# Kernel optimization log

Hardware: AMD Instinct MI355X
Metric: run time of the kernel (lower is better)

Reference implementation:

```python
import jax, jax.numpy as jnp
import numpy as np

N = 4096
TAU = 0.2          # args.tau relaxation temperature
EPS = 1e-10        # numerical guard for logit of clamped probs


def setup_inputs() -> dict:
    key = jax.random.key(0)
    k1, k2, k3 = jax.random.split(key, 3)
    r = jax.random.uniform(k1, (N, N))
    ori_adj = jnp.where(r < 0.005, -1.0, jnp.where(r < 0.01, 1.0, 0.0)).astype(jnp.float32)
    # nn.init.uniform_(change_links_prob, 0.0, 0.001)
    change_links_prob = jax.random.uniform(k2, (N, N), minval=0.0, maxval=0.001, dtype=jnp.float32)
    # uniform noise for the RelaxedBernoulli logistic reparameterization
    u = jax.random.uniform(k3, (N, N), minval=1e-6, maxval=1.0 - 1e-6, dtype=jnp.float32)
    return {"ori_adj": ori_adj, "change_links_prob": change_links_prob, "u": u}


def reference(ori_adj, change_links_prob, u):
    # --- get_modified_adj: RelaxedBernoulliStraightThrough(tau, clamp(p,0,1)).rsample() ---
    p = jnp.clip(change_links_prob, EPS, 1.0 - EPS)      # torch.clamp(p, 0, 1) + logit guard
    logits = jnp.log(p) - jnp.log1p(-p)
    noise = jnp.log(u) - jnp.log1p(-u)                   # logistic noise
    soft = jax.nn.sigmoid((logits + noise) / TAU)        # relaxed sample
    hard = jnp.round(soft)                               # quantized sample
    change_prob = soft + jax.lax.stop_gradient(hard - soft)  # straight-through
    mod_adj = ori_adj + change_prob * (-2.0 * ori_adj)   # ori_adj * (1 - 2*b)

    # --- balance_degree_directed(mod_adj) ---
    # torch.diag(matrix) returns the diagonal VECTOR, broadcast-subtracted per row (faithful).
    A = mod_adj + mod_adj.T - jnp.diag(mod_adj)
    A_abs = jnp.abs(A)
    tr3 = jnp.einsum('ij,jk,ki->', A, A, A)              # trace(A @ A @ A)
    tr3_abs = jnp.einsum('ij,jk,ki->', A_abs, A_abs, A_abs)
    balance = 0.5 * (1.0 + tr3 / tr3_abs)
    return mod_adj, balance
```

## Files before the change

kernel.cpp:

```cpp
#include <hip/hip_runtime.h>
#include <hip/hip_bf16.h>
#include <cstdint>
#include <cstddef>

#define N 4096
#define NN ((size_t)N * (size_t)N)

typedef int   int4v   __attribute__((ext_vector_type(4)));
typedef float float4v __attribute__((ext_vector_type(4)));

__device__ inline void async16(const void* g, void* lds) {
    __builtin_amdgcn_global_load_lds(
        (const __attribute__((address_space(1))) void*)g,
        (__attribute__((address_space(3))) void*)lds, 16, 0, 0);
}

__global__ __launch_bounds__(512) void fused_mod_build(
        const float* __restrict__ ori,
        const float* __restrict__ clp,
        const float* __restrict__ uu,
        float* __restrict__ out,
        signed char* __restrict__ A,
        signed char* __restrict__ AT,
        signed char* __restrict__ Aa,
        signed char* __restrict__ ATa,
        double* __restrict__ accs) {
    const int I = blockIdx.x, J = blockIdx.y;
    if (I > J) return;
    __shared__ float sm1[64][65];
    __shared__ float sm2[64][65];
    __shared__ float dI[64], dJ[64];
    const int t    = threadIdx.x;
    const int half = t >> 8;
    const int tt   = t & 255;
    const int r    = tt >> 2;
    const int q    = tt & 3;
    const int bi = I * 64, bj = J * 64;
    if (I == 0 && J == 0 && t < 2) accs[t] = 0.0;
    if (t < 128) {
        const int x = (t < 64) ? (bi + t) : (bj + (t - 64));
        const size_t off = (size_t)x * N + x;
        const float o = ori[off];
        const float hard = (clp[off] + uu[off] >= 1.0f) ? 1.0f : 0.0f;
        const float d = fmaf(hard, -2.0f * o, o);
        if (t < 64) dI[t] = d; else dJ[t - 64] = d;
    }
    {
        const int rowbase = half ? bj : bi;
        const int colbase = half ? bi : bj;
        float (*sm)[65] = half ? sm2 : sm1;
        const bool wr = (half == 0) || (I != J);
        #pragma unroll
        for (int k = 0; k < 4; ++k) {
            const size_t off = (size_t)(rowbase + r) * N + colbase + k * 16 + q * 4;
            const float4v o4 = *(const float4v*)(ori + off);
            const float4v p4 = *(const float4v*)(clp + off);
            const float4v u4 = *(const float4v*)(uu + off);
            float4v m;
            #pragma unroll
            for (int c = 0; c < 4; ++c) {
                const float hard = (p4[c] + u4[c] >= 1.0f) ? 1.0f : 0.0f;
                m[c] = fmaf(hard, -2.0f * o4[c], o4[c]);
                sm[r][k * 16 + q * 4 + c] = m[c];
            }
            if (wr) *(float4v*)(out + off) = m;
        }
    }
    __syncthreads();
    if (half == 0) {
        int pkA1[4], pkAa1[4], pkT1[4], pkTa1[4];
        #pragma unroll
        for (int w = 0; w < 4; ++w) {
            int a1w = 0, aa1w = 0, t1w = 0, ta1w = 0;
            #pragma unroll
            for (int k = 0; k < 4; ++k) {
                const int c = q * 16 + w * 4 + k;
                const float a1 = sm1[r][c] + sm2[c][r] - dJ[c];
                const int v1 = (int)a1;  const int u1 = v1 < 0 ? -v1 : v1;
                a1w  |= (v1 & 255) << (8 * k);
                aa1w |= (u1 & 255) << (8 * k);
                const float t1 = sm1[c][r] + sm2[r][c] - dJ[r];
                const int w1 = (int)t1;  const int x1 = w1 < 0 ? -w1 : w1;
                t1w  |= (w1 & 255) << (8 * k);
                ta1w |= (x1 & 255) << (8 * k);
            }
            pkA1[w] = a1w; pkAa1[w] = aa1w; pkT1[w] = t1w; pkTa1[w] = ta1w;
        }
        const size_t oIJ = (size_t)(bi + r) * N + bj + q * 16;
        const size_t oJI = (size_t)(bj + r) * N + bi + q * 16;
        *(int4v*)&A  [oIJ] = *(int4v*)pkA1;
        *(int4v*)&Aa [oIJ] = *(int4v*)pkAa1;
        *(int4v*)&AT [oJI] = *(int4v*)pkT1;
        *(int4v*)&ATa[oJI] = *(int4v*)pkTa1;
    } else if (I != J) {
        int pkA2[4], pkAa2[4], pkT2[4], pkTa2[4];
        #pragma unroll
        for (int w = 0; w < 4; ++w) {
            int a2w = 0, aa2w = 0, t2w = 0, ta2w = 0;
            #pragma unroll
            for (int k = 0; k < 4; ++k) {
                const int c = q * 16 + w * 4 + k;
                const float a2 = sm2[r][c] + sm1[c][r] - dI[c];
                const int v2 = (int)a2;  const int u2 = v2 < 0 ? -v2 : v2;
                a2w  |= (v2 & 255) << (8 * k);
                aa2w |= (u2 & 255) << (8 * k);
                const float t2 = sm2[c][r] + sm1[r][c] - dI[r];
                const int w2 = (int)t2;  const int x2 = w2 < 0 ? -w2 : w2;
                t2w  |= (w2 & 255) << (8 * k);
                ta2w |= (x2 & 255) << (8 * k);
            }
            pkA2[w] = a2w; pkAa2[w] = aa2w; pkT2[w] = t2w; pkTa2[w] = ta2w;
        }
        const size_t oIJ = (size_t)(bi + r) * N + bj + q * 16;
        const size_t oJI = (size_t)(bj + r) * N + bi + q * 16;
        *(int4v*)&A  [oJI] = *(int4v*)pkA2;
        *(int4v*)&Aa [oJI] = *(int4v*)pkAa2;
        *(int4v*)&AT [oIJ] = *(int4v*)pkT2;
        *(int4v*)&ATa[oIJ] = *(int4v*)pkTa2;
    }
}

#define BK 64
#define NT (N / BK)
#define BUFSZ 32768

__global__ __launch_bounds__(512, 2) void gemm_trace_i8(
        const signed char* __restrict__ Ag,
        const signed char* __restrict__ ATg,
        const signed char* __restrict__ Aag,
        const signed char* __restrict__ ATag,
        double* __restrict__ accs) {
    __shared__ __align__(16) signed char lds[4 * BUFSZ];
    __shared__ int red[8];
    const int z = blockIdx.z;
    const signed char* Asrc = z ? Aag  : Ag;
    const signed char* Bsrc = z ? ATag : ATg;
    const int i0 = blockIdx.y * 256;
    const int k0 = blockIdx.x * 256;
    const int t = threadIdx.x;
    const int lane = t & 63;
    const int wave = t >> 6;
    const int wm = wave >> 2;
    const int wn = wave & 3;
    const int quad = lane >> 4;
    const int col  = lane & 15;

    const int c1 = t;
    const int r1 = c1 >> 2;
    const int r2 = r1 + 128;
    const int s1 = (((c1 & 3) ^ ((r1 >> 1) & 3)) << 4);
    const int s2 = (((c1 & 3) ^ ((r2 >> 1) & 3)) << 4);
    const signed char* gA1 = Asrc + (size_t)(i0 + r1) * N + s1;
    const signed char* gA2 = Asrc + (size_t)(i0 + r2) * N + s2;
    const signed char* gB1 = Bsrc + (size_t)(k0 + r1) * N + s1;
    const signed char* gB2 = Bsrc + (size_t)(k0 + r2) * N + s2;
    const int ldsA1 = (wave * 64) * 16;
    const int ldsA2 = 8192  + (wave * 64) * 16;
    const int ldsB1 = 16384 + (wave * 64) * 16;
    const int ldsB2 = 24576 + (wave * 64) * 16;
    const int fsw = ((quad ^ ((col >> 1) & 3)) << 4);

    int4v acc[8][4];
    #pragma unroll
    for (int a = 0; a < 8; ++a)
        #pragma unroll
        for (int b = 0; b < 4; ++b)
            acc[a][b] = (int4v){0, 0, 0, 0};

    for (int p = 0; p < 3; ++p) {
        const int pb = p * BUFSZ;
        const size_t go = (size_t)p * BK;
        async16(gA1 + go, lds + pb + ldsA1);
        async16(gA2 + go, lds + pb + ldsA2);
        async16(gB1 + go, lds + pb + ldsB1);
        async16(gB2 + go, lds + pb + ldsB2);
    }
    asm volatile("s_waitcnt vmcnt(8)" ::: "memory");
    __builtin_amdgcn_s_barrier();
    __builtin_amdgcn_sched_barrier(0);

    for (int j = 0; j < NT; ++j) {
        const int buf = (j & 3) * BUFSZ;
        const signed char* Ab = lds + buf;
        const signed char* Bb = lds + buf + 16384;
        const int pre = j + 3;
        const size_t go = (size_t)pre * BK;
        const int pb = (pre & 3) * BUFSZ;
        int4v af0[4], af1[4], bf[4];
        #pragma unroll
        for (int tr = 0; tr < 4; ++tr)
            af0[tr] = *(const int4v*)(Ab + ((wm * 128 + tr * 16 + col) << 6) + fsw);
        #pragma unroll
        for (int tc = 0; tc < 4; ++tc)
            bf[tc] = *(const int4v*)(Bb + ((wn * 64 + tc * 16 + col) << 6) + fsw);
        #pragma unroll
        for (int tr = 0; tr < 4; ++tr)
            af1[tr] = *(const int4v*)(Ab + ((wm * 128 + 64 + tr * 16 + col) << 6) + fsw);
        if (pre < NT) {
            async16(gA1 + go, lds + pb + ldsA1);
            async16(gA2 + go, lds + pb + ldsA2);
            async16(gB1 + go, lds + pb + ldsB1);
            async16(gB2 + go, lds + pb + ldsB2);
        }
        asm volatile("s_waitcnt lgkmcnt(4)" ::: "memory");
        __builtin_amdgcn_sched_barrier(0);
        __builtin_amdgcn_s_setprio(1);
        #pragma unroll
        for (int tr = 0; tr < 4; ++tr)
            #pragma unroll
            for (int tc = 0; tc < 4; ++tc)
                acc[tr][tc] = __builtin_amdgcn_mfma_i32_16x16x64_i8(af0[tr], bf[tc], acc[tr][tc], 0, 0, 0);
        __builtin_amdgcn_s_setprio(0);
        asm volatile("s_waitcnt lgkmcnt(0)" ::: "memory");
        __builtin_amdgcn_sched_barrier(0);
        __builtin_amdgcn_s_setprio(1);
        #pragma unroll
        for (int tr = 0; tr < 4; ++tr)
            #pragma unroll
            for (int tc = 0; tc < 4; ++tc)
                acc[4 + tr][tc] = __builtin_amdgcn_mfma_i32_16x16x64_i8(af1[tr], bf[tc], acc[4 + tr][tc], 0, 0, 0);
        __builtin_amdgcn_s_setprio(0);
        if (j < NT - 3)       { asm volatile("s_waitcnt vmcnt(8)" ::: "memory"); }
        else if (j == NT - 3) { asm volatile("s_waitcnt vmcnt(4)" ::: "memory"); }
        else if (j == NT - 2) { asm volatile("s_waitcnt vmcnt(0)" ::: "memory"); }
        __builtin_amdgcn_s_barrier();
        __builtin_amdgcn_sched_barrier(0);
    }

    int part = 0;
    #pragma unroll
    for (int mr = 0; mr < 8; ++mr) {
        const int ib = i0 + wm * 128 + mr * 16 + quad * 4;
        #pragma unroll
        for (int tc = 0; tc < 4; ++tc) {
            const int kk = k0 + wn * 64 + tc * 16 + col;
            const int mv = *(const int*)&Asrc[(size_t)kk * N + ib];
            #pragma unroll
            for (int r = 0; r < 4; ++r)
                part += acc[mr][tc][r] * (int)(signed char)(mv >> (8 * r));
        }
    }
    #pragma unroll
    for (int off = 32; off > 0; off >>= 1)
        part += __shfl_down(part, off, 64);
    if (lane == 0) red[wave] = part;
    __syncthreads();
    if (t == 0) {
        int tot = 0;
        #pragma unroll
        for (int w = 0; w < 8; ++w) tot += red[w];
        atomicAdd(&accs[z], (double)tot);
    }
}

__global__ void finalize_kernel(const double* __restrict__ accs, float* __restrict__ out) {
    out[NN] = (float)(0.5 * (1.0 + accs[0] / accs[1]));
}

extern "C" void kernel_launch(void* const* d_in, const int* in_sizes, int n_in,
                              void* d_out, int out_size, void* d_ws, size_t ws_size,
                              hipStream_t stream) {
    const float* ori = (const float*)d_in[0];
    const float* clp = (const float*)d_in[1];
    const float* u   = (const float*)d_in[2];
    float* out = (float*)d_out;
    char* ws = (char*)d_ws;
    signed char* A8   = (signed char*)ws;
    signed char* AT8  = (signed char*)(ws + NN);
    signed char* Aa8  = (signed char*)(ws + 2 * NN);
    signed char* ATa8 = (signed char*)(ws + 3 * NN);
    double*      accs = (double*)(ws + 4 * NN);

    fused_mod_build<<<dim3(64, 64), 512, 0, stream>>>(
        ori, clp, u, out, A8, AT8, Aa8, ATa8, accs);
    gemm_trace_i8<<<dim3(N / 256, N / 256, 2), 512, 0, stream>>>(A8, AT8, Aa8, ATa8, accs);
    finalize_kernel<<<1, 1, 0, stream>>>(accs, out);
}
```

Before: 393.7 us.

## Compute abs GEMM from signed int8 tiles in-register, drop separate abs matrices

The build kernel now writes only the signed int8 matrix and its transpose, not separate absolute-value copies. The GEMM kernel computes byte-wise absolute values of the loaded fragments in registers and runs both the signed and absolute MFMA chains in one pass over shared tiles. This halves global int8 writes and GEMM operand loads, and the grid drops its z dimension. In exchange it doubles the accumulator registers (launch bounds change to one block per CU), adds ALU work per fragment, and it also batches the float loads in the build kernel.

```diff
diff --git a/kernel.cpp b/kernel.cpp
--- a/kernel.cpp
+++ b/kernel.cpp
@@ -13,6 +13,20 @@
     __builtin_amdgcn_global_load_lds(
         (const __attribute__((address_space(1))) void*)g,
         (__attribute__((address_space(3))) void*)lds, 16, 0, 0);
+}
+
+__device__ inline unsigned absb4(unsigned v) {
+    unsigned s = (v >> 7) & 0x01010101u;
+    unsigned m = s * 255u;
+    return (v ^ m) + s;
+}
+__device__ inline int4v absfrag(int4v v) {
+    int4v r;
+    r[0] = (int)absb4((unsigned)v[0]);
+    r[1] = (int)absb4((unsigned)v[1]);
+    r[2] = (int)absb4((unsigned)v[2]);
+    r[3] = (int)absb4((unsigned)v[3]);
+    return r;
 }
 
 __global__ __launch_bounds__(512) void fused_mod_build(
@@ -22,8 +36,6 @@
         float* __restrict__ out,
         signed char* __restrict__ A,
         signed char* __restrict__ AT,
-        signed char* __restrict__ Aa,
-        signed char* __restrict__ ATa,
         double* __restrict__ accs) {
     const int I = blockIdx.x, J = blockIdx.y;
     if (I > J) return;
@@ -50,73 +62,80 @@
         const int colbase = half ? bi : bj;
         float (*sm)[65] = half ? sm2 : sm1;
         const bool wr = (half == 0) || (I != J);
+        float4v o4[4], p4[4], u4[4];
         #pragma unroll
         for (int k = 0; k < 4; ++k) {
             const size_t off = (size_t)(rowbase + r) * N + colbase + k * 16 + q * 4;
-            const float4v o4 = *(const float4v*)(ori + off);
-            const float4v p4 = *(const float4v*)(clp + off);
-            const float4v u4 = *(const float4v*)(uu + off);
+            o4[k] = *(const float4v*)(ori + off);
+        }
+        #pragma unroll
+        for (int k = 0; k < 4; ++k) {
+            const size_t off = (size_t)(rowbase + r) * N + colbase + k * 16 + q * 4;
+            p4[k] = *(const float4v*)(clp + off);
+        }
+        #pragma unroll
+        for (int k = 0; k < 4; ++k) {
+            const size_t off = (size_t)(rowbase + r) * N + colbase + k * 16 + q * 4;
+            u4[k] = *(const float4v*)(uu + off);
+        }
+        #pragma unroll
+        for (int k = 0; k < 4; ++k) {
             float4v m;
             #pragma unroll
             for (int c = 0; c < 4; ++c) {
-                const float hard = (p4[c] + u4[c] >= 1.0f) ? 1.0f : 0.0f;
-                m[c] = fmaf(hard, -2.0f * o4[c], o4[c]);
+                const float hard = (p4[k][c] + u4[k][c] >= 1.0f) ? 1.0f : 0.0f;
+                m[c] = fmaf(hard, -2.0f * o4[k][c], o4[k][c]);
                 sm[r][k * 16 + q * 4 + c] = m[c];
             }
-            if (wr) *(float4v*)(out + off) = m;
+            if (wr) {
+                const size_t off = (size_t)(rowbase + r) * N + colbase + k * 16 + q * 4;
+                *(float4v*)(out + off) = m;
+            }
         }
     }
     __syncthreads();
     if (half == 0) {
-        int pkA1[4], pkAa1[4], pkT1[4], pkTa1[4];
+        int pkA1[4], pkT1[4];
         #pragma unroll
         for (int w = 0; w < 4; ++w) {
-            int a1w = 0, aa1w = 0, t1w = 0, ta1w = 0;
+            int a1w = 0, t1w = 0;
             #pragma unroll
             for (int k = 0; k < 4; ++k) {
                 const int c = q * 16 + w * 4 + k;
                 const float a1 = sm1[r][c] + sm2[c][r] - dJ[c];
-                const int v1 = (int)a1;  const int u1 = v1 < 0 ? -v1 : v1;
-                a1w  |= (v1 & 255) << (8 * k);
-                aa1w |= (u1 & 255) << (8 * k);
+                const int v1 = (int)a1;
+                a1w |= (v1 & 255) << (8 * k);
                 const float t1 = sm1[c][r] + sm2[r][c] - dJ[r];
-                const int w1 = (int)t1;  const int x1 = w1 < 0 ? -w1 : w1;
-                t1w  |= (w1 & 255) << (8 * k);
-                ta1w |= (x1 & 255) << (8 * k);
-            }
-            pkA1[w] = a1w; pkAa1[w] = aa1w; pkT1[w] = t1w; pkTa1[w] = ta1w;
+                const int w1 = (int)t1;
+                t1w |= (w1 & 255) << (8 * k);
+            }
+            pkA1[w] = a1w; pkT1[w] = t1w;
         }
         const size_t oIJ = (size_t)(bi + r) * N + bj + q * 16;
         const size_t oJI = (size_t)(bj + r) * N + bi + q * 16;
-        *(int4v*)&A  [oIJ] = *(int4v*)pkA1;
-        *(int4v*)&Aa [oIJ] = *(int4v*)pkAa1;
-        *(int4v*)&AT [oJI] = *(int4v*)pkT1;
-        *(int4v*)&ATa[oJI] = *(int4v*)pkTa1;
+        *(int4v*)&A [oIJ] = *(int4v*)pkA1;
+        *(int4v*)&AT[oJI] = *(int4v*)pkT1;
     } else if (I != J) {
-        int pkA2[4], pkAa2[4], pkT2[4], pkTa2[4];
+        int pkA2[4], pkT2[4];
         #pragma unroll
         for (int w = 0; w < 4; ++w) {
-            int a2w = 0, aa2w = 0, t2w = 0, ta2w = 0;
+            int a2w = 0, t2w = 0;
             #pragma unroll
             for (int k = 0; k < 4; ++k) {
                 const int c = q * 16 + w * 4 + k;
                 const float a2 = sm2[r][c] + sm1[c][r] - dI[c];
-                const int v2 = (int)a2;  const int u2 = v2 < 0 ? -v2 : v2;
-                a2w  |= (v2 & 255) << (8 * k);
-                aa2w |= (u2 & 255) << (8 * k);
+                const int v2 = (int)a2;
+                a2w |= (v2 & 255) << (8 * k);
                 const float t2 = sm2[c][r] + sm1[r][c] - dI[r];
-                const int w2 = (int)t2;  const int x2 = w2 < 0 ? -w2 : w2;
-                t2w  |= (w2 & 255) << (8 * k);
-                ta2w |= (x2 & 255) << (8 * k);
-            }
-            pkA2[w] = a2w; pkAa2[w] = aa2w; pkT2[w] = t2w; pkTa2[w] = ta2w;
+                const int w2 = (int)t2;
+                t2w |= (w2 & 255) << (8 * k);
+            }
+            pkA2[w] = a2w; pkT2[w] = t2w;
         }
         const size_t oIJ = (size_t)(bi + r) * N + bj + q * 16;
         const size_t oJI = (size_t)(bj + r) * N + bi + q * 16;
-        *(int4v*)&A  [oJI] = *(int4v*)pkA2;
-        *(int4v*)&Aa [oJI] = *(int4v*)pkAa2;
-        *(int4v*)&AT [oIJ] = *(int4v*)pkT2;
-        *(int4v*)&ATa[oIJ] = *(int4v*)pkTa2;
+        *(int4v*)&A [oJI] = *(int4v*)pkA2;
+        *(int4v*)&AT[oIJ] = *(int4v*)pkT2;
     }
 }
 
@@ -124,17 +143,14 @@
 #define NT (N / BK)
 #define BUFSZ 32768
 
-__global__ __launch_bounds__(512, 2) void gemm_trace_i8(
+__global__ __launch_bounds__(512, 1) void gemm_trace_i8(
         const signed char* __restrict__ Ag,
         const signed char* __restrict__ ATg,
-        const signed char* __restrict__ Aag,
-        const signed char* __restrict__ ATag,
         double* __restrict__ accs) {
     __shared__ __align__(16) signed char lds[4 * BUFSZ];
-    __shared__ int red[8];
-    const int z = blockIdx.z;
-    const signed char* Asrc = z ? Aag  : Ag;
-    const signed char* Bsrc = z ? ATag : ATg;
+    __shared__ int red[8][2];
+    const signed char* Asrc = Ag;
+    const signed char* Bsrc = ATg;
     const int i0 = blockIdx.y * 256;
     const int k0 = blockIdx.x * 256;
     const int t = threadIdx.x;
@@ -160,12 +176,14 @@
     const int ldsB2 = 24576 + (wave * 64) * 16;
     const int fsw = ((quad ^ ((col >> 1) & 3)) << 4);
 
-    int4v acc[8][4];
+    int4v accA[8][4], accB[8][4];
     #pragma unroll
     for (int a = 0; a < 8; ++a)
         #pragma unroll
-        for (int b = 0; b < 4; ++b)
-            acc[a][b] = (int4v){0, 0, 0, 0};
+        for (int b = 0; b < 4; ++b) {
+            accA[a][b] = (int4v){0, 0, 0, 0};
+            accB[a][b] = (int4v){0, 0, 0, 0};
+        }
 
     for (int p = 0; p < 3; ++p) {
         const int pb = p * BUFSZ;
@@ -205,20 +223,33 @@
         asm volatile("s_waitcnt lgkmcnt(4)" ::: "memory");
         __builtin_amdgcn_sched_barrier(0);
         __builtin_amdgcn_s_setprio(1);
-        #pragma unroll
-        for (int tr = 0; tr < 4; ++tr)
-            #pragma unroll
-            for (int tc = 0; tc < 4; ++tc)
-                acc[tr][tc] = __builtin_amdgcn_mfma_i32_16x16x64_i8(af0[tr], bf[tc], acc[tr][tc], 0, 0, 0);
-        __builtin_amdgcn_s_setprio(0);
-        asm volatile("s_waitcnt lgkmcnt(0)" ::: "memory");
-        __builtin_amdgcn_sched_barrier(0);
-        __builtin_amdgcn_s_setprio(1);
-        #pragma unroll
-        for (int tr = 0; tr < 4; ++tr)
-            #pragma unroll
-            for (int tc = 0; tc < 4; ++tc)
-                acc[4 + tr][tc] = __builtin_amdgcn_mfma_i32_16x16x64_i8(af1[tr], bf[tc], acc[4 + tr][tc], 0, 0, 0);
+        {
+            int4v ab[4];
+            #pragma unroll
+            for (int tc = 0; tc < 4; ++tc) ab[tc] = absfrag(bf[tc]);
+            #pragma unroll
+            for (int tr = 0; tr < 4; ++tr) {
+                const int4v aa = absfrag(af0[tr]);
+                #pragma unroll
+                for (int tc = 0; tc < 4; ++tc) {
+                    accA[tr][tc] = __builtin_amdgcn_mfma_i32_16x16x64_i8(af0[tr], bf[tc], accA[tr][tc], 0, 0, 0);
+                    accB[tr][tc] = __builtin_amdgcn_mfma_i32_16x16x64_i8(aa,      ab[tc], accB[tr][tc], 0, 0, 0);
+                }
+            }
+            __builtin_amdgcn_s_setprio(0);
+            asm volatile("s_waitcnt lgkmcnt(0)" ::: "memory");
+            __builtin_amdgcn_sched_barrier(0);
+            __builtin_amdgcn_s_setprio(1);
+            #pragma unroll
+            for (int tr = 0; tr < 4; ++tr) {
+                const int4v aa = absfrag(af1[tr]);
+                #pragma unroll
+                for (int tc = 0; tc < 4; ++tc) {
+                    accA[4 + tr][tc] = __builtin_amdgcn_mfma_i32_16x16x64_i8(af1[tr], bf[tc], accA[4 + tr][tc], 0, 0, 0);
+                    accB[4 + tr][tc] = __builtin_amdgcn_mfma_i32_16x16x64_i8(aa,      ab[tc], accB[4 + tr][tc], 0, 0, 0);
+                }
+            }
+        }
         __builtin_amdgcn_s_setprio(0);
         if (j < NT - 3)       { asm volatile("s_waitcnt vmcnt(8)" ::: "memory"); }
         else if (j == NT - 3) { asm volatile("s_waitcnt vmcnt(4)" ::: "memory"); }
@@ -227,29 +258,35 @@
         __builtin_amdgcn_sched_barrier(0);
     }
 
-    int part = 0;
+    int partA = 0, partB = 0;
     #pragma unroll
     for (int mr = 0; mr < 8; ++mr) {
         const int ib = i0 + wm * 128 + mr * 16 + quad * 4;
         #pragma unroll
         for (int tc = 0; tc < 4; ++tc) {
             const int kk = k0 + wn * 64 + tc * 16 + col;
-            const int mv = *(const int*)&Asrc[(size_t)kk * N + ib];
-            #pragma unroll
-            for (int r = 0; r < 4; ++r)
-                part += acc[mr][tc][r] * (int)(signed char)(mv >> (8 * r));
+            const unsigned mv = *(const unsigned*)&Asrc[(size_t)kk * N + ib];
+            const unsigned av = absb4(mv);
+            #pragma unroll
+            for (int r = 0; r < 4; ++r) {
+                partA += accA[mr][tc][r] * (int)(signed char)(mv >> (8 * r));
+                partB += accB[mr][tc][r] * (int)(signed char)(av >> (8 * r));
+            }
         }
     }
     #pragma unroll
-    for (int off = 32; off > 0; off >>= 1)
-        part += __shfl_down(part, off, 64);
-    if (lane == 0) red[wave] = part;
+    for (int off = 32; off > 0; off >>= 1) {
+        partA += __shfl_down(partA, off, 64);
+        partB += __shfl_down(partB, off, 64);
+    }
+    if (lane == 0) { red[wave][0] = partA; red[wave][1] = partB; }
     __syncthreads();
     if (t == 0) {
-        int tot = 0;
-        #pragma unroll
-        for (int w = 0; w < 8; ++w) tot += red[w];
-        atomicAdd(&accs[z], (double)tot);
+        int totA = 0, totB = 0;
+        #pragma unroll
+        for (int w = 0; w < 8; ++w) { totA += red[w][0]; totB += red[w][1]; }
+        atomicAdd(&accs[0], (double)totA);
+        atomicAdd(&accs[1], (double)totB);
     }
 }
 
@@ -265,14 +302,12 @@
     const float* u   = (const float*)d_in[2];
     float* out = (float*)d_out;
     char* ws = (char*)d_ws;
-    signed char* A8   = (signed char*)ws;
-    signed char* AT8  = (signed char*)(ws + NN);
-    signed char* Aa8  = (signed char*)(ws + 2 * NN);
-    signed char* ATa8 = (signed char*)(ws + 3 * NN);
-    double*      accs = (double*)(ws + 4 * NN);
+    signed char* A8  = (signed char*)ws;
+    signed char* AT8 = (signed char*)(ws + NN);
+    double*      accs = (double*)(ws + 2 * NN);
 
     fused_mod_build<<<dim3(64, 64), 512, 0, stream>>>(
-        ori, clp, u, out, A8, AT8, Aa8, ATa8, accs);
-    gemm_trace_i8<<<dim3(N / 256, N / 256, 2), 512, 0, stream>>>(A8, AT8, Aa8, ATa8, accs);
+        ori, clp, u, out, A8, AT8, accs);
+    gemm_trace_i8<<<dim3(N / 256, N / 256), 512, 0, stream>>>(A8, AT8, accs);
     finalize_kernel<<<1, 1, 0, stream>>>(accs, out);
 }
```

Result: slower. 1.045 ms (+165.5%).

## Split elementwise mod pass from int8 build and fold finalize into GEMM

Applied to the files above, without the earlier changes.

The fused build kernel is split in two. A streaming kernel computes mod_adj, writes the output and extracts the diagonal. A full-grid 64x64 block kernel then re-reads the output to build the int8 A, AT and abs matrices, with the abs computed by a packed-byte bit trick. The triangular-grid symmetry trick is dropped, so each tile is read once more from the fp32 output instead of from the three inputs. The separate finalize kernel is removed and replaced by a last-block atomic counter inside the GEMM, saving one launch. Total global traffic goes up, since the output is written then re-read and the build grid is no longer halved.

```diff
diff --git a/kernel.cpp b/kernel.cpp
--- a/kernel.cpp
+++ b/kernel.cpp
@@ -15,108 +15,107 @@
         (__attribute__((address_space(3))) void*)lds, 16, 0, 0);
 }
 
-__global__ __launch_bounds__(512) void fused_mod_build(
-        const float* __restrict__ ori,
-        const float* __restrict__ clp,
-        const float* __restrict__ uu,
-        float* __restrict__ out,
+__device__ inline unsigned absb4(unsigned v) {
+    unsigned s = (v >> 7) & 0x01010101u;
+    unsigned m = s * 255u;
+    return (v ^ m) + s;
+}
+
+__global__ void mod_diag(const float* __restrict__ ori,
+                         const float* __restrict__ clp,
+                         const float* __restrict__ uu,
+                         float* __restrict__ out,
+                         float* __restrict__ diag,
+                         double* __restrict__ accs) {
+    if (blockIdx.x == 0 && threadIdx.x == 0) {
+        accs[0] = 0.0; accs[1] = 0.0;
+        *(unsigned*)(accs + 2) = 0u;
+    }
+    size_t i = ((size_t)blockIdx.x * blockDim.x + threadIdx.x) * 4;
+    const float4v p4 = *(const float4v*)(clp + i);
+    const float4v u4 = *(const float4v*)(uu + i);
+    const float4v o4 = *(const float4v*)(ori + i);
+    float4v r;
+    #pragma unroll
+    for (int c = 0; c < 4; ++c) {
+        float hard = (p4[c] + u4[c] >= 1.0f) ? 1.0f : 0.0f;
+        r[c] = fmaf(hard, -2.0f * o4[c], o4[c]);
+    }
+    *(float4v*)(out + i) = r;
+    const int row  = (int)(i >> 12);
+    const int drel = row - (int)(i & 4095);
+    if (drel >= 0 && drel < 4) diag[row] = r[drel];
+}
+
+__global__ __launch_bounds__(512) void build64(
+        const float* __restrict__ out,
+        const float* __restrict__ diag,
         signed char* __restrict__ A,
         signed char* __restrict__ AT,
         signed char* __restrict__ Aa,
-        signed char* __restrict__ ATa,
-        double* __restrict__ accs) {
-    const int I = blockIdx.x, J = blockIdx.y;
-    if (I > J) return;
+        signed char* __restrict__ ATa) {
     __shared__ float sm1[64][65];
     __shared__ float sm2[64][65];
-    __shared__ float dI[64], dJ[64];
+    __shared__ float dJ[64];
+    const int I = blockIdx.x, J = blockIdx.y;
+    const int bi = I * 64, bj = J * 64;
     const int t    = threadIdx.x;
     const int half = t >> 8;
     const int tt   = t & 255;
     const int r    = tt >> 2;
     const int q    = tt & 3;
-    const int bi = I * 64, bj = J * 64;
-    if (I == 0 && J == 0 && t < 2) accs[t] = 0.0;
-    if (t < 128) {
-        const int x = (t < 64) ? (bi + t) : (bj + (t - 64));
-        const size_t off = (size_t)x * N + x;
-        const float o = ori[off];
-        const float hard = (clp[off] + uu[off] >= 1.0f) ? 1.0f : 0.0f;
-        const float d = fmaf(hard, -2.0f * o, o);
-        if (t < 64) dI[t] = d; else dJ[t - 64] = d;
-    }
+    if (t < 64) dJ[t] = diag[bj + t];
     {
         const int rowbase = half ? bj : bi;
         const int colbase = half ? bi : bj;
         float (*sm)[65] = half ? sm2 : sm1;
-        const bool wr = (half == 0) || (I != J);
         #pragma unroll
         for (int k = 0; k < 4; ++k) {
             const size_t off = (size_t)(rowbase + r) * N + colbase + k * 16 + q * 4;
-            const float4v o4 = *(const float4v*)(ori + off);
-            const float4v p4 = *(const float4v*)(clp + off);
-            const float4v u4 = *(const float4v*)(uu + off);
-            float4v m;
-            #pragma unroll
-            for (int c = 0; c < 4; ++c) {
-                const float hard = (p4[c] + u4[c] >= 1.0f) ? 1.0f : 0.0f;
-                m[c] = fmaf(hard, -2.0f * o4[c], o4[c]);
-                sm[r][k * 16 + q * 4 + c] = m[c];
-            }
-            if (wr) *(float4v*)(out + off) = m;
+            const float4v v = *(const float4v*)(out + off);
+            sm[r][k * 16 + q * 4 + 0] = v[0];
+            sm[r][k * 16 + q * 4 + 1] = v[1];
+            sm[r][k * 16 + q * 4 + 2] = v[2];
+            sm[r][k * 16 + q * 4 + 3] = v[3];
         }
     }
     __syncthreads();
     if (half == 0) {
-        int pkA1[4], pkAa1[4], pkT1[4], pkTa1[4];
+        int pkA[4], pkAb[4];
         #pragma unroll
         for (int w = 0; w < 4; ++w) {
-            int a1w = 0, aa1w = 0, t1w = 0, ta1w = 0;
+            int aw = 0;
             #pragma unroll
             for (int k = 0; k < 4; ++k) {
                 const int c = q * 16 + w * 4 + k;
-                const float a1 = sm1[r][c] + sm2[c][r] - dJ[c];
-                const int v1 = (int)a1;  const int u1 = v1 < 0 ? -v1 : v1;
-                a1w  |= (v1 & 255) << (8 * k);
-                aa1w |= (u1 & 255) << (8 * k);
-                const float t1 = sm1[c][r] + sm2[r][c] - dJ[r];
-                const int w1 = (int)t1;  const int x1 = w1 < 0 ? -w1 : w1;
-                t1w  |= (w1 & 255) << (8 * k);
-                ta1w |= (x1 & 255) << (8 * k);
+                const float a = sm1[r][c] + sm2[c][r] - dJ[c];
+                const int v = (int)a;
+                aw |= (v & 255) << (8 * k);
             }
-            pkA1[w] = a1w; pkAa1[w] = aa1w; pkT1[w] = t1w; pkTa1[w] = ta1w;
+            pkA[w] = aw;
+            pkAb[w] = (int)absb4((unsigned)aw);
         }
         const size_t oIJ = (size_t)(bi + r) * N + bj + q * 16;
-        const size_t oJI = (size_t)(bj + r) * N + bi + q * 16;
-        *(int4v*)&A  [oIJ] = *(int4v*)pkA1;
-        *(int4v*)&Aa [oIJ] = *(int4v*)pkAa1;
-        *(int4v*)&AT [oJI] = *(int4v*)pkT1;
-        *(int4v*)&ATa[oJI] = *(int4v*)pkTa1;
-    } else if (I != J) {
-        int pkA2[4], pkAa2[4], pkT2[4], pkTa2[4];
+        *(int4v*)&A [oIJ] = *(int4v*)pkA;
+        *(int4v*)&Aa[oIJ] = *(int4v*)pkAb;
+    } else {
+        int pkT[4], pkTb[4];
         #pragma unroll
         for (int w = 0; w < 4; ++w) {
-            int a2w = 0, aa2w = 0, t2w = 0, ta2w = 0;
+            int tw = 0;
             #pragma unroll
             for (int k = 0; k < 4; ++k) {
                 const int c = q * 16 + w * 4 + k;
-                const float a2 = sm2[r][c] + sm1[c][r] - dI[c];
-                const int v2 = (int)a2;  const int u2 = v2 < 0 ? -v2 : v2;
-                a2w  |= (v2 & 255) << (8 * k);
-                aa2w |= (u2 & 255) << (8 * k);
-                const float t2 = sm2[c][r] + sm1[r][c] - dI[r];
-                const int w2 = (int)t2;  const int x2 = w2 < 0 ? -w2 : w2;
-                t2w  |= (w2 & 255) << (8 * k);
-                ta2w |= (x2 & 255) << (8 * k);
+                const float a = sm1[c][r] + sm2[r][c] - dJ[r];
+                const int v = (int)a;
+                tw |= (v & 255) << (8 * k);
             }
-            pkA2[w] = a2w; pkAa2[w] = aa2w; pkT2[w] = t2w; pkTa2[w] = ta2w;
-        }
-        const size_t oIJ = (size_t)(bi + r) * N + bj + q * 16;
+            pkT[w] = tw;
+            pkTb[w] = (int)absb4((unsigned)tw);
+        }
         const size_t oJI = (size_t)(bj + r) * N + bi + q * 16;
-        *(int4v*)&A  [oJI] = *(int4v*)pkA2;
-        *(int4v*)&Aa [oJI] = *(int4v*)pkAa2;
-        *(int4v*)&AT [oIJ] = *(int4v*)pkT2;
-        *(int4v*)&ATa[oIJ] = *(int4v*)pkTa2;
+        *(int4v*)&AT [oJI] = *(int4v*)pkT;
+        *(int4v*)&ATa[oJI] = *(int4v*)pkTb;
     }
 }
 
@@ -129,7 +128,8 @@
         const signed char* __restrict__ ATg,
         const signed char* __restrict__ Aag,
         const signed char* __restrict__ ATag,
-        double* __restrict__ accs) {
+        double* __restrict__ accs,
+        float* __restrict__ outbal) {
     __shared__ __align__(16) signed char lds[4 * BUFSZ];
     __shared__ int red[8];
     const int z = blockIdx.z;
@@ -234,7 +234,8 @@
         #pragma unroll
         for (int tc = 0; tc < 4; ++tc) {
             const int kk = k0 + wn * 64 + tc * 16 + col;
-            const int mv = *(const int*)&Asrc[(size_t)kk * N + ib];
+            const int mv = *(const int*)&Bsrc[(size_t)(i0 + wm * 128 + mr * 16 + quad * 4) * 0 + 0] * 0
+                         + *(const int*)&Asrc[(size_t)kk * N + ib];
             #pragma unroll
             for (int r = 0; r < 4; ++r)
                 part += acc[mr][tc][r] * (int)(signed char)(mv >> (8 * r));
@@ -250,11 +251,14 @@
         #pragma unroll
         for (int w = 0; w < 8; ++w) tot += red[w];
         atomicAdd(&accs[z], (double)tot);
-    }
-}
-
-__global__ void finalize_kernel(const double* __restrict__ accs, float* __restrict__ out) {
-    out[NN] = (float)(0.5 * (1.0 + accs[0] / accs[1]));
+        __threadfence();
+        unsigned* cnt = (unsigned*)(accs + 2);
+        const unsigned old = atomicAdd(cnt, 1u);
+        if (old == 2u * (N / 256) * (N / 256) - 1u) {
+            __threadfence();
+            outbal[NN] = (float)(0.5 * (1.0 + accs[0] / accs[1]));
+        }
+    }
 }
 
 extern "C" void kernel_launch(void* const* d_in, const int* in_sizes, int n_in,
@@ -269,10 +273,10 @@
     signed char* AT8  = (signed char*)(ws + NN);
     signed char* Aa8  = (signed char*)(ws + 2 * NN);
     signed char* ATa8 = (signed char*)(ws + 3 * NN);
-    double*      accs = (double*)(ws + 4 * NN);
-
-    fused_mod_build<<<dim3(64, 64), 512, 0, stream>>>(
-        ori, clp, u, out, A8, AT8, Aa8, ATa8, accs);
-    gemm_trace_i8<<<dim3(N / 256, N / 256, 2), 512, 0, stream>>>(A8, AT8, Aa8, ATa8, accs);
-    finalize_kernel<<<1, 1, 0, stream>>>(accs, out);
-}
+    float*       diag = (float*)(ws + 4 * NN);
+    double*      accs = (double*)(ws + 4 * NN + 4096 * 4);
+
+    mod_diag<<<dim3((unsigned)(NN / 1024)), 256, 0, stream>>>(ori, clp, u, out, diag, accs);
+    build64<<<dim3(64, 64), 512, 0, stream>>>(out, diag, A8, AT8, Aa8, ATa8);
+    gemm_trace_i8<<<dim3(N / 256, N / 256, 2), 512, 0, stream>>>(A8, AT8, Aa8, ATa8, accs, out);
+}
```

New measurement: 364.4 us. 1.08x faster.
